# Performance work log

Hardware: AMD Instinct MI355X
Metric: run time of the kernel (lower is better)

Reference implementation:

```python
import jax, jax.numpy as jnp
import numpy as np

N_NODES = 1500
E = 48000
IN = 128
OUT = 32
HEADS = 4
EDIM = 16


def setup_inputs() -> dict:
    key = jax.random.key(0)
    ks = jax.random.split(key, 16)
    rn = lambda k, shape, s=0.1: jax.random.normal(k, shape, dtype=jnp.float32) * s
    return {
        "x": jax.random.normal(ks[0], (N_NODES, IN), dtype=jnp.float32),
        "edges": jax.random.randint(ks[1], (2, E), 0, N_NODES),
        "edge_feature": jax.random.normal(ks[2], (E, EDIM), dtype=jnp.float32),
        "W1": rn(ks[3], (IN, HEADS * OUT)),
        "att_src1": rn(ks[4], (HEADS, OUT)),
        "att_dst1": rn(ks[5], (HEADS, OUT)),
        "We": rn(ks[6], (EDIM, HEADS * OUT)),
        "att_e": rn(ks[7], (HEADS, OUT)),
        "b1": jnp.zeros((OUT,), jnp.float32),
        "W2": rn(ks[8], (OUT, HEADS * OUT)),
        "att_src2": rn(ks[9], (HEADS, OUT)),
        "att_dst2": rn(ks[10], (HEADS, OUT)),
        "b2": jnp.zeros((OUT,), jnp.float32),
        "fc1_w": rn(ks[11], (2 * OUT, 32)),
        "fc1_b": jnp.zeros((32,), jnp.float32),
        "fc2_w": rn(ks[12], (32, 2)),
        "fc2_b": jnp.zeros((2,), jnp.float32),
    }


def _gat(h, src, dst, n, a_src, a_dst, bias, extra_alpha=None):
    # h: [n, H, C] projected node features; edges j=src -> i=dst (PyG GATConv)
    alpha = (h * a_src).sum(-1)[src] + (h * a_dst).sum(-1)[dst]  # [Etot, H]
    if extra_alpha is not None:
        alpha = alpha + extra_alpha
    alpha = jax.nn.leaky_relu(alpha, negative_slope=0.2)
    m = jax.ops.segment_max(alpha, dst, num_segments=n)  # per-dst softmax (stable)
    e = jnp.exp(alpha - m[dst])
    s = jax.ops.segment_sum(e, dst, num_segments=n)
    w = e / s[dst]  # every node has a self loop -> denom > 0
    out = jax.ops.segment_sum(w[:, :, None] * h[src], dst, num_segments=n)  # [n, H, C]
    return out.mean(axis=1) + bias  # concat=False -> mean over heads


def reference(x, edges, edge_feature, W1, att_src1, att_dst1, We, att_e, b1,
              W2, att_src2, att_dst2, b2, fc1_w, fc1_b, fc2_w, fc2_b):
    n = x.shape[0]
    src0, dst0 = edges[0], edges[1]
    loop = jnp.arange(n, dtype=src0.dtype)
    src = jnp.concatenate([src0, loop])
    dst = jnp.concatenate([dst0, loop])
    # add_self_loops fill_value='mean': self-loop attr = mean of incoming edge attrs
    cnt = jax.ops.segment_sum(jnp.ones_like(dst0, dtype=jnp.float32), dst0, num_segments=n)
    loop_attr = jax.ops.segment_sum(edge_feature, dst0, num_segments=n) / jnp.maximum(cnt, 1.0)[:, None]
    ea = jnp.concatenate([edge_feature, loop_attr], axis=0)  # [E+n, EDIM]

    H, C = att_src1.shape
    # layer 1: GATConv with edge features
    h1 = (x @ W1).reshape(n, H, C)
    extra = ((ea @ We).reshape(-1, H, C) * att_e).sum(-1)  # [E+n, H]
    x1 = _gat(h1, src, dst, n, att_src1, att_dst1, b1, extra)  # [n, OUT]
    # layer 2: GATConv without edge features
    h2 = (x1 @ W2).reshape(n, H, C)
    x2 = _gat(h2, src, dst, n, att_src2, att_dst2, b2)  # [n, OUT]

    # per-edge gather-concat into a (n^2, 2*OUT) buffer; rows >= E stay zero,
    # exactly as the original Python loop leaves them
    pair = jnp.concatenate([x2[src0], x2[dst0]], axis=1)  # [E, 2*OUT]
    x_edges = jnp.zeros((n * n, 2 * C), dtype=x2.dtype).at[jnp.arange(src0.shape[0])].set(pair)
    hcls = jax.nn.relu(x_edges @ fc1_w + fc1_b)
    return jax.nn.softmax(hcls @ fc2_w + fc2_b, axis=1)
```

## Files before the change

kernel.cpp:

```cpp
#include <hip/hip_runtime.h>
#include <cmath>

#define N_NODES 1500
#define NE 48000
#define IN_DIM 128
#define OUT_DIM 32
#define HEADS 4
#define HC 128
#define EDIM 16
#define SLOTS 96
#define NFL4 (((N_NODES * N_NODES - NE) * 2) / 4)
#define PBASE 0xAAAAAAAAu
#define GRID 512

typedef float nf4 __attribute__((ext_vector_type(4)));

__device__ __forceinline__ float comp4(float4 v, int h) {
    float a = (h & 1) ? v.y : v.x;
    float b = (h & 1) ? v.w : v.z;
    return (h & 2) ? b : a;
}
__device__ __forceinline__ float lk(float a) { return a > 0.f ? a : 0.2f * a; }

__device__ __forceinline__ int xcc_id() {
    int x;
    asm volatile("s_getreg_b32 %0, hwreg(HW_REG_XCC_ID)" : "=s"(x));
    return x & 7;
}

__device__ __forceinline__ float4 fill_const(
        const float* fc1b, const float* fc2w, const float* fc2b) {
    float l0 = fc2b[0], l1 = fc2b[1];
    #pragma unroll
    for (int j = 0; j < 32; ++j) {
        float a = fmaxf(fc1b[j], 0.f);
        l0 = fmaf(a, fc2w[2 * j], l0);
        l1 = fmaf(a, fc2w[2 * j + 1], l1);
    }
    float mx = fmaxf(l0, l1);
    float e0 = __expf(l0 - mx), e1 = __expf(l1 - mx);
    float inv = 1.f / (e0 + e1);
    return make_float4(e0 * inv, e1 * inv, e0 * inv, e1 * inv);
}

__device__ __forceinline__ void gridbar(unsigned* __restrict__ bws, unsigned phase) {
    __syncthreads();
    if (threadIdx.x == 0) {
        const int xcc = xcc_id();
        unsigned* a = &bws[((phase - 1u) * 8u + (unsigned)xcc) * 16u];
        bool lead = (__hip_atomic_fetch_add(a, 1u, __ATOMIC_RELAXED,
                                            __HIP_MEMORY_SCOPE_AGENT) == PBASE);
        if (lead) {
            for (;;) {
                unsigned ssum = 0;
                #pragma unroll
                for (int q = 0; q < 8; ++q)
                    ssum += __hip_atomic_load(&bws[((phase - 1u) * 8u + q) * 16u],
                                              __ATOMIC_RELAXED,
                                              __HIP_MEMORY_SCOPE_AGENT) - PBASE;
                if (ssum >= (unsigned)GRID) break;
                __builtin_amdgcn_s_sleep(1);
            }
            __builtin_amdgcn_fence(__ATOMIC_RELEASE, "agent");
            unsigned nblk = __hip_atomic_load(a, __ATOMIC_RELAXED,
                                              __HIP_MEMORY_SCOPE_AGENT) - PBASE;
            unsigned* fin = &bws[384u + (phase - 1u) * 16u];
            __hip_atomic_fetch_add(fin, nblk, __ATOMIC_RELAXED,
                                   __HIP_MEMORY_SCOPE_AGENT);
            while ((int)(__hip_atomic_load(fin, __ATOMIC_RELAXED,
                         __HIP_MEMORY_SCOPE_AGENT) - (PBASE + (unsigned)GRID)) < 0)
                __builtin_amdgcn_s_sleep(1);
            __builtin_amdgcn_fence(__ATOMIC_ACQUIRE, "agent");
            asm volatile("s_waitcnt vmcnt(0)" ::: "memory");
            __hip_atomic_store(&bws[432u + (unsigned)xcc * 16u], PBASE + phase,
                               __ATOMIC_RELAXED, __HIP_MEMORY_SCOPE_AGENT);
        } else {
            while ((int)(__hip_atomic_load(&bws[432u + (unsigned)xcc * 16u],
                         __ATOMIC_RELAXED, __HIP_MEMORY_SCOPE_AGENT)
                         - (PBASE + phase)) < 0)
                __builtin_amdgcn_s_sleep(2);
        }
    }
    __syncthreads();
}

template <int MODE>
__device__ __forceinline__ void gat_wave(
        int i, const float* __restrict__ h, const float* __restrict__ asrc,
        const float* __restrict__ adst, const float* __restrict__ ext,
        const int* __restrict__ csr_src, const int* __restrict__ deg,
        const float* __restrict__ bias,
        const float* __restrict__ Wn, const float* __restrict__ a_s2,
        const float* __restrict__ a_d2, float* h2o, float* asrc2,
        float* adst2, float* uvo, int* sns_w, float* swt_w)
{
    const int lane = threadIdx.x & 63;
    const int head = lane >> 4;
    const int p = lane & 15;
    int dg = (int)((unsigned)deg[i] - PBASE);
    if (dg > SLOTS) dg = SLOTS;
    const int base = i * SLOTS;
    const float4 ad4 = *(const float4*)&adst[i * 4];
    const float* hb = h + 2 * lane;

    float4 m = make_float4(-INFINITY, -INFINITY, -INFINITY, -INFINITY);
    float4 s = make_float4(0.f, 0.f, 0.f, 0.f);
    float4 sx = make_float4(0.f, 0.f, 0.f, 0.f);
    float2 acc = make_float2(0.f, 0.f);

    for (int pos = 0; pos < dg; pos += 64) {
        int cnt = dg - pos; if (cnt > 64) cnt = 64;
        bool act = lane < cnt;
        int sn = 0;
        float4 al = make_float4(-INFINITY, -INFINITY, -INFINITY, -INFINITY);
        if (act) {
            sn = csr_src[base + pos + lane];
            float4 a4 = *(const float4*)&asrc[sn * 4];
            al = make_float4(a4.x + ad4.x, a4.y + ad4.y, a4.z + ad4.z, a4.w + ad4.w);
            if (MODE == 1) {
                float4 e4 = *(const float4*)&ext[(base + pos + lane) * 4];
                al.x += e4.x; al.y += e4.y; al.z += e4.z; al.w += e4.w;
                sx.x += e4.x; sx.y += e4.y; sx.z += e4.z; sx.w += e4.w;
            }
            al.x = lk(al.x); al.y = lk(al.y); al.z = lk(al.z); al.w = lk(al.w);
        }
        float4 cm = al;
        #pragma unroll
        for (int o = 32; o >= 1; o >>= 1) {
            cm.x = fmaxf(cm.x, __shfl_xor(cm.x, o));
            cm.y = fmaxf(cm.y, __shfl_xor(cm.y, o));
            cm.z = fmaxf(cm.z, __shfl_xor(cm.z, o));
            cm.w = fmaxf(cm.w, __shfl_xor(cm.w, o));
        }
        float4 mn = make_float4(fmaxf(m.x, cm.x), fmaxf(m.y, cm.y),
                                fmaxf(m.z, cm.z), fmaxf(m.w, cm.w));
        float4 r = make_float4(__expf(m.x - mn.x), __expf(m.y - mn.y),
                               __expf(m.z - mn.z), __expf(m.w - mn.w));
        float4 wv4 = make_float4(0.f, 0.f, 0.f, 0.f);
        if (act) {
            wv4.x = __expf(al.x - mn.x); wv4.y = __expf(al.y - mn.y);
            wv4.z = __expf(al.z - mn.z); wv4.w = __expf(al.w - mn.w);
        }
        float4 cs = wv4;
        #pragma unroll
        for (int o = 32; o >= 1; o >>= 1) {
            cs.x += __shfl_xor(cs.x, o); cs.y += __shfl_xor(cs.y, o);
            cs.z += __shfl_xor(cs.z, o); cs.w += __shfl_xor(cs.w, o);
        }
        s = make_float4(s.x * r.x + cs.x, s.y * r.y + cs.y,
                        s.z * r.z + cs.z, s.w * r.w + cs.w);
        float rh = comp4(r, head);
        acc.x *= rh; acc.y *= rh;
        m = mn;
        if (act) {
            sns_w[lane] = sn;
            *(float4*)&swt_w[lane * 4] = wv4;
        }
        int jj = 0;
        for (; jj + 8 <= cnt; jj += 8) {
            int s0 = sns_w[jj], s1 = sns_w[jj+1], s2 = sns_w[jj+2], s3 = sns_w[jj+3];
            int s4 = sns_w[jj+4], s5 = sns_w[jj+5], s6 = sns_w[jj+6], s7 = sns_w[jj+7];
            float w0 = swt_w[(jj)*4+head],   w1 = swt_w[(jj+1)*4+head];
            float w2 = swt_w[(jj+2)*4+head], w3 = swt_w[(jj+3)*4+head];
            float w4 = swt_w[(jj+4)*4+head], w5 = swt_w[(jj+5)*4+head];
            float w6 = swt_w[(jj+6)*4+head], w7 = swt_w[(jj+7)*4+head];
            float2 h0 = *(const float2*)&hb[s0 * HC], h1 = *(const float2*)&hb[s1 * HC];
            float2 h2 = *(const float2*)&hb[s2 * HC], h3 = *(const float2*)&hb[s3 * HC];
            float2 h4 = *(const float2*)&hb[s4 * HC], h5 = *(const float2*)&hb[s5 * HC];
            float2 h6 = *(const float2*)&hb[s6 * HC], h7 = *(const float2*)&hb[s7 * HC];
            acc.x = fmaf(w0, h0.x, acc.x); acc.y = fmaf(w0, h0.y, acc.y);
            acc.x = fmaf(w1, h1.x, acc.x); acc.y = fmaf(w1, h1.y, acc.y);
            acc.x = fmaf(w2, h2.x, acc.x); acc.y = fmaf(w2, h2.y, acc.y);
            acc.x = fmaf(w3, h3.x, acc.x); acc.y = fmaf(w3, h3.y, acc.y);
            acc.x = fmaf(w4, h4.x, acc.x); acc.y = fmaf(w4, h4.y, acc.y);
            acc.x = fmaf(w5, h5.x, acc.x); acc.y = fmaf(w5, h5.y, acc.y);
            acc.x = fmaf(w6, h6.x, acc.x); acc.y = fmaf(w6, h6.y, acc.y);
            acc.x = fmaf(w7, h7.x, acc.x); acc.y = fmaf(w7, h7.y, acc.y);
        }
        for (; jj < cnt; ++jj) {
            int sj = sns_w[jj];
            float wj = swt_w[jj * 4 + head];
            float2 hv = *(const float2*)&hb[sj * HC];
            acc.x = fmaf(wj, hv.x, acc.x);
            acc.y = fmaf(wj, hv.y, acc.y);
        }
    }
    {
        float4 a4 = *(const float4*)&asrc[i * 4];
        float4 al = make_float4(a4.x + ad4.x, a4.y + ad4.y, a4.z + ad4.z, a4.w + ad4.w);
        if (MODE == 1) {
            #pragma unroll
            for (int o = 32; o >= 1; o >>= 1) {
                sx.x += __shfl_xor(sx.x, o); sx.y += __shfl_xor(sx.y, o);
                sx.z += __shfl_xor(sx.z, o); sx.w += __shfl_xor(sx.w, o);
            }
            float invc = 1.f / (float)(dg > 1 ? dg : 1);
            al.x = fmaf(sx.x, invc, al.x); al.y = fmaf(sx.y, invc, al.y);
            al.z = fmaf(sx.z, invc, al.z); al.w = fmaf(sx.w, invc, al.w);
        }
        al.x = lk(al.x); al.y = lk(al.y); al.z = lk(al.z); al.w = lk(al.w);
        float4 mn = make_float4(fmaxf(m.x, al.x), fmaxf(m.y, al.y),
                                fmaxf(m.z, al.z), fmaxf(m.w, al.w));
        float4 r = make_float4(__expf(m.x - mn.x), __expf(m.y - mn.y),
                               __expf(m.z - mn.z), __expf(m.w - mn.w));
        float4 wv4 = make_float4(__expf(al.x - mn.x), __expf(al.y - mn.y),
                                 __expf(al.z - mn.z), __expf(al.w - mn.w));
        s = make_float4(s.x * r.x + wv4.x, s.y * r.y + wv4.y,
                        s.z * r.z + wv4.z, s.w * r.w + wv4.w);
        float rh = comp4(r, head), wh = comp4(wv4, head);
        float2 hv = *(const float2*)&hb[i * HC];
        acc.x = acc.x * rh + wh * hv.x;
        acc.y = acc.y * rh + wh * hv.y;
    }
    float sh = comp4(s, head);
    float2 v = make_float2(acc.x / sh, acc.y / sh);
    v.x += __shfl_xor(v.x, 16); v.y += __shfl_xor(v.y, 16);
    v.x += __shfl_xor(v.x, 32); v.y += __shfl_xor(v.y, 32);
    float2 bp = *(const float2*)&bias[2 * p];
    float2 xr = make_float2(0.25f * v.x + bp.x, 0.25f * v.y + bp.y);

    if (MODE == 1) {
        float2 a2 = make_float2(0.f, 0.f);
        #pragma unroll
        for (int k = 0; k < OUT_DIM; ++k) {
            float xk = __shfl((k & 1) ? xr.y : xr.x, k >> 1);
            float2 wr = *(const float2*)&Wn[k * HC + 2 * lane];
            a2.x = fmaf(xk, wr.x, a2.x);
            a2.y = fmaf(xk, wr.y, a2.y);
        }
        *(float2*)&h2o[i * HC + 2 * lane] = a2;
        float2 s2 = *(const float2*)&a_s2[2 * lane];
        float2 d2 = *(const float2*)&a_d2[2 * lane];
        float lps = a2.x * s2.x + a2.y * s2.y;
        float lpd = a2.x * d2.x + a2.y * d2.y;
        #pragma unroll
        for (int o = 8; o >= 1; o >>= 1) {
            lps += __shfl_xor(lps, o);
            lpd += __shfl_xor(lpd, o);
        }
        if (p == 0) {
            asrc2[i * 4 + head] = lps;
            adst2[i * 4 + head] = lpd;
        }
    } else {
        if (lane < 32) {
            bool isv = lane >= 16;
            int j0 = isv ? (2 * lane - 32) : (2 * lane);
            float2 a2 = make_float2(0.f, 0.f);
            #pragma unroll
            for (int k = 0; k < OUT_DIM; ++k) {
                float xk = __shfl((k & 1) ? xr.y : xr.x, k >> 1);
                int row = isv ? (OUT_DIM + k) : k;
                float2 wr = *(const float2*)&Wn[row * 32 + j0];
                a2.x = fmaf(xk, wr.x, a2.x);
                a2.y = fmaf(xk, wr.y, a2.y);
            }
            *(float2*)&uvo[i * 64 + 2 * lane] = a2;
        }
    }
}

__global__ __launch_bounds__(256, 2) void k_fused(
    const float* __restrict__ x, const int* __restrict__ edges,
    const float* __restrict__ ef,
    const float* __restrict__ W1, const float* __restrict__ as1,
    const float* __restrict__ ad1, const float* __restrict__ We,
    const float* __restrict__ ate, const float* __restrict__ b1,
    const float* __restrict__ W2, const float* __restrict__ as2,
    const float* __restrict__ ad2, const float* __restrict__ b2,
    const float* __restrict__ fc1w, const float* __restrict__ fc1b,
    const float* __restrict__ fc2w, const float* __restrict__ fc2b,
    float* __restrict__ out,
    float* __restrict__ h1, float* __restrict__ asrc1, float* __restrict__ adst1,
    int* __restrict__ csr_src, float* __restrict__ csr_ext, int* __restrict__ deg,
    float* __restrict__ h2v, float* __restrict__ asrc2, float* __restrict__ adst2,
    float* __restrict__ uv, unsigned* __restrict__ bws)
{
    const int t = threadIdx.x;
    const int b = blockIdx.x;
    const int* src = edges;
    const int* dst = edges + NE;
    __shared__ float P[EDIM * HEADS];
    __shared__ float xs[6 * IN_DIM];
    __shared__ int   sns[4][SLOTS];
    __shared__ float swt[4][SLOTS * 4];

    if (b < 188) {
        if (t < EDIM * HEADS) {
            int k = t >> 2, hh = t & 3;
            float a = 0.f;
            #pragma unroll
            for (int c = 0; c < OUT_DIM; ++c)
                a = fmaf(We[k * HC + hh * OUT_DIM + c], ate[hh * OUT_DIM + c], a);
            P[t] = a;
        }
        __syncthreads();
        int e = b * 256 + t;
        if (e < NE) {
            int d = dst[e];
            unsigned r = (unsigned)atomicAdd(&deg[d], 1) - PBASE;
            const float4* efp = (const float4*)&ef[e * EDIM];
            float er[16];
            float4 f;
            f = efp[0]; er[0]=f.x; er[1]=f.y; er[2]=f.z; er[3]=f.w;
            f = efp[1]; er[4]=f.x; er[5]=f.y; er[6]=f.z; er[7]=f.w;
            f = efp[2]; er[8]=f.x; er[9]=f.y; er[10]=f.z; er[11]=f.w;
            f = efp[3]; er[12]=f.x; er[13]=f.y; er[14]=f.z; er[15]=f.w;
            float a0=0.f, a1=0.f, a2=0.f, a3=0.f;
            #pragma unroll
            for (int k = 0; k < EDIM; ++k) {
                a0 = fmaf(er[k], P[k*4+0], a0);
                a1 = fmaf(er[k], P[k*4+1], a1);
                a2 = fmaf(er[k], P[k*4+2], a2);
                a3 = fmaf(er[k], P[k*4+3], a3);
            }
            if (r < SLOTS) {
                int slot = d * SLOTS + (int)r;
                csr_src[slot] = src[e];
                *(float4*)&csr_ext[slot * 4] = make_float4(a0, a1, a2, a3);
            }
        }
    } else if (b < 438) {
        int i0 = 6 * (b - 188);
        for (int idx = t; idx < 6 * IN_DIM; idx += 256) xs[idx] = x[i0 * IN_DIM + idx];
        __syncthreads();
        int col = t & 127, g = t >> 7;
        float a0 = 0.f, a1 = 0.f, a2 = 0.f;
        for (int k = 0; k < IN_DIM; ++k) {
            float w = W1[k * HC + col];
            a0 = fmaf(xs[(g * 3 + 0) * IN_DIM + k], w, a0);
            a1 = fmaf(xs[(g * 3 + 1) * IN_DIM + k], w, a1);
            a2 = fmaf(xs[(g * 3 + 2) * IN_DIM + k], w, a2);
        }
        float as = as1[col], ad = ad1[col];
        int hh = col >> 5, c = col & 31;
        float av[3] = {a0, a1, a2};
        #pragma unroll
        for (int r = 0; r < 3; ++r) {
            int node = i0 + g * 3 + r;
            h1[node * HC + col] = av[r];
            float ps = av[r] * as, pd = av[r] * ad;
            #pragma unroll
            for (int o = 16; o >= 1; o >>= 1) { ps += __shfl_down(ps, o, 32); pd += __shfl_down(pd, o, 32); }
            if (c == 0) { asrc1[node * 4 + hh] = ps; adst1[node * 4 + hh] = pd; }
        }
    }
    {
        float4 qv = fill_const(fc1b, fc2w, fc2b);
        nf4 q = {qv.x, qv.y, qv.z, qv.w};
        nf4* o4 = (nf4*)(out + NE * 2);
        for (int idx = b * 256 + t; idx < NFL4; idx += GRID * 256)
            __builtin_nontemporal_store(q, &o4[idx]);
    }
    gridbar(bws, 1);

    {
        const int wid = t >> 6;
        int i = wid * GRID + b;
        if (i < N_NODES)
            gat_wave<1>(i, h1, asrc1, adst1, csr_ext, csr_src, deg, b1,
                        W2, as2, ad2, h2v, asrc2, adst2, nullptr,
                        sns[wid], swt[wid]);
    }
    gridbar(bws, 2);

    {
        const int wid = t >> 6;
        int i = wid * GRID + b;
        if (i < N_NODES)
            gat_wave<2>(i, h2v, asrc2, adst2, nullptr, csr_src, deg, b2,
                        fc1w, nullptr, nullptr, nullptr, nullptr, nullptr, uv,
                        sns[wid], swt[wid]);
    }
    gridbar(bws, 3);

    int gid = b * 256 + t;
    if (gid < NE) {
        int e = gid;
        int si = src[e], di = dst[e];
        const float4* up = (const float4*)&uv[si * 64];
        const float4* vp = (const float4*)&uv[di * 64 + 32];
        float l0 = fc2b[0], l1 = fc2b[1];
        #pragma unroll
        for (int q = 0; q < 8; ++q) {
            float4 u4 = up[q], v4 = vp[q];
            float a;
            a = fmaxf(u4.x + v4.x + fc1b[4*q+0], 0.f); l0 = fmaf(a, fc2w[8*q+0], l0); l1 = fmaf(a, fc2w[8*q+1], l1);
            a = fmaxf(u4.y + v4.y + fc1b[4*q+1], 0.f); l0 = fmaf(a, fc2w[8*q+2], l0); l1 = fmaf(a, fc2w[8*q+3], l1);
            a = fmaxf(u4.z + v4.z + fc1b[4*q+2], 0.f); l0 = fmaf(a, fc2w[8*q+4], l0); l1 = fmaf(a, fc2w[8*q+5], l1);
            a = fmaxf(u4.w + v4.w + fc1b[4*q+3], 0.f); l0 = fmaf(a, fc2w[8*q+6], l0); l1 = fmaf(a, fc2w[8*q+7], l1);
        }
        float mx = fmaxf(l0, l1);
        float e0 = __expf(l0 - mx), e1 = __expf(l1 - mx);
        float inv = 1.f / (e0 + e1);
        *(float2*)&out[2 * e] = make_float2(e0 * inv, e1 * inv);
    }
}

extern "C" void kernel_launch(void* const* d_in, const int* in_sizes, int n_in,
                              void* d_out, int out_size, void* d_ws, size_t ws_size,
                              hipStream_t stream) {
    (void)in_sizes; (void)n_in; (void)out_size; (void)ws_size;
    const float* x    = (const float*)d_in[0];
    const int*  edges = (const int*)d_in[1];
    const float* ef   = (const float*)d_in[2];
    const float* W1   = (const float*)d_in[3];
    const float* as1  = (const float*)d_in[4];
    const float* ad1  = (const float*)d_in[5];
    const float* We   = (const float*)d_in[6];
    const float* ate  = (const float*)d_in[7];
    const float* b1   = (const float*)d_in[8];
    const float* W2   = (const float*)d_in[9];
    const float* as2  = (const float*)d_in[10];
    const float* ad2  = (const float*)d_in[11];
    const float* b2   = (const float*)d_in[12];
    const float* fc1w = (const float*)d_in[13];
    const float* fc1b = (const float*)d_in[14];
    const float* fc2w = (const float*)d_in[15];
    const float* fc2b = (const float*)d_in[16];
    float* out = (float*)d_out;

    char* w = (char*)d_ws;
    auto alloc = [&](size_t bytes) -> char* {
        char* p = w;
        w += (bytes + 255) & ~(size_t)255;
        return p;
    };
    float* h1      = (float*)alloc((size_t)N_NODES * HC * 4);
    float* asrc1   = (float*)alloc((size_t)N_NODES * HEADS * 4);
    float* adst1   = (float*)alloc((size_t)N_NODES * HEADS * 4);
    int*   csr_src = (int*)  alloc((size_t)N_NODES * SLOTS * 4);
    float* csr_ext = (float*)alloc((size_t)N_NODES * SLOTS * 16);
    float* h2      = (float*)alloc((size_t)N_NODES * HC * 4);
    float* asrc2   = (float*)alloc((size_t)N_NODES * HEADS * 4);
    float* adst2   = (float*)alloc((size_t)N_NODES * HEADS * 4);
    float* uv      = (float*)alloc((size_t)N_NODES * 64 * 4);
    int*   deg     = (int*)  alloc((size_t)N_NODES * 4);
    unsigned* bws  = (unsigned*)alloc(4096);

    k_fused<<<GRID, 256, 0, stream>>>(x, edges, ef, W1, as1, ad1, We, ate, b1,
                                      W2, as2, ad2, b2, fc1w, fc1b, fc2w, fc2b,
                                      out, h1, asrc1, adst1, csr_src, csr_ext,
                                      deg, h2, asrc2, adst2, uv, bws);
}
```

Baseline: 137.8 us.

## Replace grid-barrier fence/finish round with agent-scope atomic stores for shared data

Removes the second barrier round from the grid barrier: the release fence, the global finish counter and the acquire fence. In exchange, every cross-block intermediate (h1, attention logits, CSR slots, h2, uv) is written with relaxed agent-scope atomic stores, so the writes should be visible across XCCs without an explicit fence. This cuts barrier latency per phase but depends on relaxed atomics for cross-XCC ordering, which is a correctness risk. The atomic stores may also be slower than ordinary vector stores.

```diff
diff --git a/kernel.cpp b/kernel.cpp
--- a/kernel.cpp
+++ b/kernel.cpp
@@ -26,6 +26,21 @@
     int x;
     asm volatile("s_getreg_b32 %0, hwreg(HW_REG_XCC_ID)" : "=s"(x));
     return x & 7;
+}
+
+__device__ __forceinline__ void wt32(float* p, float v) {
+    __hip_atomic_store((unsigned*)p, __float_as_uint(v),
+                       __ATOMIC_RELAXED, __HIP_MEMORY_SCOPE_AGENT);
+}
+__device__ __forceinline__ void wt32i(int* p, int v) {
+    __hip_atomic_store((unsigned*)p, (unsigned)v,
+                       __ATOMIC_RELAXED, __HIP_MEMORY_SCOPE_AGENT);
+}
+__device__ __forceinline__ void wt64(float* p, float x, float y) {
+    unsigned long long u = ((unsigned long long)__float_as_uint(y) << 32)
+                         | (unsigned long long)__float_as_uint(x);
+    __hip_atomic_store((unsigned long long*)p, u,
+                       __ATOMIC_RELAXED, __HIP_MEMORY_SCOPE_AGENT);
 }
 
 __device__ __forceinline__ float4 fill_const(
@@ -61,17 +76,6 @@
                 if (ssum >= (unsigned)GRID) break;
                 __builtin_amdgcn_s_sleep(1);
             }
-            __builtin_amdgcn_fence(__ATOMIC_RELEASE, "agent");
-            unsigned nblk = __hip_atomic_load(a, __ATOMIC_RELAXED,
-                                              __HIP_MEMORY_SCOPE_AGENT) - PBASE;
-            unsigned* fin = &bws[384u + (phase - 1u) * 16u];
-            __hip_atomic_fetch_add(fin, nblk, __ATOMIC_RELAXED,
-                                   __HIP_MEMORY_SCOPE_AGENT);
-            while ((int)(__hip_atomic_load(fin, __ATOMIC_RELAXED,
-                         __HIP_MEMORY_SCOPE_AGENT) - (PBASE + (unsigned)GRID)) < 0)
-                __builtin_amdgcn_s_sleep(1);
-            __builtin_amdgcn_fence(__ATOMIC_ACQUIRE, "agent");
-            asm volatile("s_waitcnt vmcnt(0)" ::: "memory");
             __hip_atomic_store(&bws[432u + (unsigned)xcc * 16u], PBASE + phase,
                                __ATOMIC_RELAXED, __HIP_MEMORY_SCOPE_AGENT);
         } else {
@@ -228,7 +232,7 @@
             a2.x = fmaf(xk, wr.x, a2.x);
             a2.y = fmaf(xk, wr.y, a2.y);
         }
-        *(float2*)&h2o[i * HC + 2 * lane] = a2;
+        wt64(&h2o[i * HC + 2 * lane], a2.x, a2.y);
         float2 s2 = *(const float2*)&a_s2[2 * lane];
         float2 d2 = *(const float2*)&a_d2[2 * lane];
         float lps = a2.x * s2.x + a2.y * s2.y;
@@ -239,8 +243,8 @@
             lpd += __shfl_xor(lpd, o);
         }
         if (p == 0) {
-            asrc2[i * 4 + head] = lps;
-            adst2[i * 4 + head] = lpd;
+            wt32(&asrc2[i * 4 + head], lps);
+            wt32(&adst2[i * 4 + head], lpd);
         }
     } else {
         if (lane < 32) {
@@ -255,7 +259,7 @@
                 a2.x = fmaf(xk, wr.x, a2.x);
                 a2.y = fmaf(xk, wr.y, a2.y);
             }
-            *(float2*)&uvo[i * 64 + 2 * lane] = a2;
+            wt64(&uvo[i * 64 + 2 * lane], a2.x, a2.y);
         }
     }
 }
@@ -316,8 +320,9 @@
             }
             if (r < SLOTS) {
                 int slot = d * SLOTS + (int)r;
-                csr_src[slot] = src[e];
-                *(float4*)&csr_ext[slot * 4] = make_float4(a0, a1, a2, a3);
+                wt32i(&csr_src[slot], src[e]);
+                wt64(&csr_ext[slot * 4 + 0], a0, a1);
+                wt64(&csr_ext[slot * 4 + 2], a2, a3);
             }
         }
     } else if (b < 438) {
@@ -338,11 +343,14 @@
         #pragma unroll
         for (int r = 0; r < 3; ++r) {
             int node = i0 + g * 3 + r;
-            h1[node * HC + col] = av[r];
+            wt32(&h1[node * HC + col], av[r]);
             float ps = av[r] * as, pd = av[r] * ad;
             #pragma unroll
             for (int o = 16; o >= 1; o >>= 1) { ps += __shfl_down(ps, o, 32); pd += __shfl_down(pd, o, 32); }
-            if (c == 0) { asrc1[node * 4 + hh] = ps; adst1[node * 4 + hh] = pd; }
+            if (c == 0) {
+                wt32(&asrc1[node * 4 + hh], ps);
+                wt32(&adst1[node * 4 + hh], pd);
+            }
         }
     }
     {
```

New measurement: 134.2 us. -2.6%, faster.
